# Kernel optimization log

Hardware: AMD Instinct MI355X
Metric: run time of the kernel (lower is better)

Reference implementation:

```python
import jax, jax.numpy as jnp
import numpy as np

N_NODES = 50000
N_EDGES = 800000
D_IN = 128
D_OUT = 128
K = 3


def setup_inputs() -> dict:
    key = jax.random.key(0)
    k1, k2, k3, k4 = jax.random.split(key, 4)
    x = jax.random.normal(k1, (N_NODES, D_IN), dtype=jnp.float32)
    src = jax.random.randint(k2, (N_EDGES,), 0, N_NODES, dtype=jnp.int32)
    dst = jax.random.randint(k3, (N_EDGES,), 0, N_NODES, dtype=jnp.int32)
    edge_index = jnp.stack([src, dst], axis=0)  # [2, E]
    W = jax.random.normal(k4, (D_OUT, D_IN * (K + 1)), dtype=jnp.float32) * 0.02
    b = jnp.zeros((D_OUT,), dtype=jnp.float32)
    return {"x": x, "edge_index": edge_index, "W": W, "b": b}


def _mean_propagate(h, src, dst, n_nodes):
    # scatter-mean: out[v] = mean_{(u,v) in E} h[u]
    msgs = h[src]                                             # [E, D] gather
    summed = jax.ops.segment_sum(msgs, dst, num_segments=n_nodes)
    cnt = jax.ops.segment_sum(jnp.ones((src.shape[0], 1), h.dtype), dst,
                              num_segments=n_nodes)
    return summed / jnp.maximum(cnt, 1.0)


def reference(x, edge_index, W, b):
    src, dst = edge_index[0], edge_index[1]
    n = x.shape[0]
    terms = [x]
    terms.append(_mean_propagate(x, src, dst, n))             # T1 = P x
    for _ in range(K - 1):                                    # T_k = 2 P T_{k-1} - T_{k-2}
        terms.append(2.0 * _mean_propagate(terms[-1], src, dst, n) - terms[-2])
    h = jnp.concatenate(terms, axis=-1)                       # [N, D*(K+1)]
    return h @ W.T + b
```

## Files before the change

### kernel.cpp

```cpp
#include <hip/hip_runtime.h>
#include <stdint.h>

#define D 128
#define LDHB 512
#define MAXD 64
#define FILL_SUB 128

typedef unsigned short u16;
typedef __attribute__((ext_vector_type(8))) short short8;
typedef __attribute__((ext_vector_type(4))) float f32x4;

__device__ __forceinline__ u16 f2bf(float f) {
    uint32_t u = __builtin_bit_cast(uint32_t, f);
    u += 0x7FFFu + ((u >> 16) & 1u);
    return (u16)(u >> 16);
}
__device__ __forceinline__ float bflo(uint32_t w) {
    return __builtin_bit_cast(float, w << 16);
}
__device__ __forceinline__ float bfhi(uint32_t w) {
    return __builtin_bit_cast(float, w & 0xFFFF0000u);
}
__device__ __forceinline__ uint32_t packbf(float lo, float hi) {
    return (uint32_t)f2bf(lo) | ((uint32_t)f2bf(hi) << 16);
}


__global__ void zero_kernel(int* __restrict__ p, int n) {
    int i = blockIdx.x * blockDim.x + threadIdx.x;
    if (i < n) p[i] = 0;
}

__global__ __launch_bounds__(256) void fill_ell_kernel(
        const int* __restrict__ src, const int* __restrict__ dst, int E, int n,
        int* __restrict__ cnt, u16* __restrict__ ell) {
    int grp = blockIdx.x & 7;
    int sub = blockIdx.x >> 3;
    int S = (n + 7) >> 3;
    int lo = grp * S;
    int hi = lo + S; if (hi > n) hi = n;
    const int stride = FILL_SUB * 256;
    for (int i = sub * 256 + (int)threadIdx.x; i < E; i += stride) {
        int d = dst[i];
        if (d >= lo && d < hi) {
            int pos = atomicAdd(&cnt[d], 1);
            if (pos < MAXD) ell[(size_t)d * MAXD + pos] = (u16)src[i];
        }
    }
}


__global__ __launch_bounds__(256) void castx_kernel(const float* __restrict__ x,
                                                    u16* __restrict__ Hb, int n) {
    int gid = blockIdx.x * 256 + threadIdx.x;
    if (gid >= n * 16) return;
    int row = gid >> 4, c8 = (gid & 15) * 8;
    const float4* p = (const float4*)(x + (size_t)row * D + c8);
    float4 f0 = p[0], f1 = p[1];
    uint4 o;
    o.x = packbf(f0.x, f0.y); o.y = packbf(f0.z, f0.w);
    o.z = packbf(f1.x, f1.y); o.w = packbf(f1.z, f1.w);
    *(uint4*)(Hb + (size_t)row * LDHB + c8) = o;
}


__global__ __launch_bounds__(256) void packw_kernel(const float* __restrict__ W,
                                                    u16* __restrict__ Bp) {
    int o = blockIdx.x * 256 + threadIdx.x;
    int kt = o >> 13, rem = o & 8191;
    int j = rem >> 6, w = rem & 63, s2 = w >> 3, e = w & 7;
    int k16 = s2 ^ (j & 7);
    int k = kt * 64 + k16 * 8 + e;
    float val;
    if (k < 128)      val = W[(size_t)j * 512 + k];
    else if (k < 256) val = W[(size_t)j * 512 + k] - W[(size_t)j * 512 + k + 256];
    else if (k < 384) val = W[(size_t)j * 512 + k];
    else              val = 2.0f * W[(size_t)j * 512 + k];
    Bp[o] = f2bf(val);
}


__global__ __launch_bounds__(256) void prop_kernel(u16* Hb, int colin, int colsub,
                                                   float scale, int dosub,
                                                   const int* __restrict__ cnt,
                                                   const u16* __restrict__ ell,
                                                   int colout, int n) {
    int g = blockIdx.x * 16 + ((int)threadIdx.x >> 4);
    if (g >= n) return;
    int lane16 = (int)threadIdx.x & 15;
    int c8 = lane16 * 8;
    int deg = cnt[g];
    if (deg > MAXD) deg = MAXD;
    const u16* row = ell + (size_t)g * MAXD;
    float a0 = 0, a1 = 0, a2 = 0, a3 = 0, a4 = 0, a5 = 0, a6 = 0, a7 = 0;
    for (int base = 0; base < deg; base += 16) {
        int m = deg - base; if (m > 16) m = 16;
        int si = 0;
        if (lane16 < m) si = (int)row[base + lane16];
#pragma unroll 4
        for (int j = 0; j < m; ++j) {
            int s = __shfl(si, j, 16);
            uint4 v = *(const uint4*)(Hb + (size_t)s * LDHB + colin + c8);
            a0 += bflo(v.x); a1 += bfhi(v.x);
            a2 += bflo(v.y); a3 += bfhi(v.y);
            a4 += bflo(v.z); a5 += bfhi(v.z);
            a6 += bflo(v.w); a7 += bfhi(v.w);
        }
    }
    float inv = scale / (float)(deg > 1 ? deg : 1);
    a0 *= inv; a1 *= inv; a2 *= inv; a3 *= inv;
    a4 *= inv; a5 *= inv; a6 *= inv; a7 *= inv;
    if (dosub) {
        uint4 sv = *(const uint4*)(Hb + (size_t)g * LDHB + colsub + c8);
        a0 -= bflo(sv.x); a1 -= bfhi(sv.x);
        a2 -= bflo(sv.y); a3 -= bfhi(sv.y);
        a4 -= bflo(sv.z); a5 -= bfhi(sv.z);
        a6 -= bflo(sv.w); a7 -= bfhi(sv.w);
    }
    uint4 o;
    o.x = packbf(a0, a1); o.y = packbf(a2, a3);
    o.z = packbf(a4, a5); o.w = packbf(a6, a7);
    *(uint4*)(Hb + (size_t)g * LDHB + colout + c8) = o;
}


__global__ __launch_bounds__(256) void gemm_kernel(const u16* __restrict__ Hb,
                                                   const u16* __restrict__ Bp,
                                                   const float* __restrict__ bias,
                                                   float* __restrict__ out, int n) {
    __shared__ uint4 Asm[128 * 8];
    __shared__ uint4 Bsm[128 * 8];

    const int t = (int)threadIdx.x;
    const int wave = t >> 6, lane = t & 63;
    const int wr = wave >> 1, wc = wave & 1;
    const int m0 = blockIdx.x * 128;
    const int lrow = lane & 15, lk = lane >> 4;

    f32x4 acc[4][4];
#pragma unroll
    for (int m = 0; m < 4; ++m)
#pragma unroll
        for (int nf = 0; nf < 4; ++nf) acc[m][nf] = (f32x4)0.0f;

#pragma unroll 1
    for (int kt = 0; kt < 8; ++kt) {
#pragma unroll
        for (int i = 0; i < 4; ++i) {
            int flat = i * 256 + t;
            int row = flat >> 3, c16 = flat & 7;
            int grow = m0 + row;
            uint4 v = make_uint4(0, 0, 0, 0);
            if (grow < n) v = *(const uint4*)(Hb + (size_t)grow * LDHB + kt * 64 + c16 * 8);
            Asm[row * 8 + (c16 ^ (row & 7))] = v;
        }
        const u16* bsrc = Bp + kt * 8192;
#pragma unroll
        for (int i = 0; i < 4; ++i) {
            int flat = i * 256 + t;
            Bsm[flat] = *(const uint4*)(bsrc + flat * 8);
        }
        __syncthreads();

#pragma unroll
        for (int kk2 = 0; kk2 < 2; ++kk2) {
            int k16 = kk2 * 4 + lk;
            short8 af[4], bfv[4];
#pragma unroll
            for (int m = 0; m < 4; ++m) {
                int r = wr * 64 + m * 16 + lrow;
                af[m] = __builtin_bit_cast(short8, Asm[r * 8 + (k16 ^ (r & 7))]);
            }
#pragma unroll
            for (int nf = 0; nf < 4; ++nf) {
                int j = wc * 64 + nf * 16 + lrow;
                bfv[nf] = __builtin_bit_cast(short8, Bsm[j * 8 + (k16 ^ (j & 7))]);
            }
#pragma unroll
            for (int m = 0; m < 4; ++m)
#pragma unroll
                for (int nf = 0; nf < 4; ++nf)
                    acc[m][nf] = __builtin_amdgcn_mfma_f32_16x16x32_bf16(
                        af[m], bfv[nf], acc[m][nf], 0, 0, 0);
        }
        __syncthreads();
    }

#pragma unroll
    for (int nf = 0; nf < 4; ++nf) {
        int j = wc * 64 + nf * 16 + lrow;
        float bj = bias[j];
#pragma unroll
        for (int m = 0; m < 4; ++m) {
            int rbase = m0 + wr * 64 + m * 16 + lk * 4;
#pragma unroll
            for (int q = 0; q < 4; ++q) {
                int row = rbase + q;
                if (row < n) out[(size_t)row * D + j] = acc[m][nf][q] + bj;
            }
        }
    }
}


static inline size_t align_up(size_t x, size_t a) { return (x + a - 1) & ~(a - 1); }

extern "C" void kernel_launch(void* const* d_in, const int* in_sizes, int n_in,
                              void* d_out, int out_size, void* d_ws, size_t ws_size,
                              hipStream_t stream) {
    const float* x  = (const float*)d_in[0];
    const int*   ei = (const int*)d_in[1];
    const float* W  = (const float*)d_in[2];
    const float* b  = (const float*)d_in[3];
    float* out = (float*)d_out;

    const int n = in_sizes[0] / D;
    const int E = in_sizes[1] / 2;
    const int* src = ei;
    const int* dst = ei + E;

    char* w = (char*)d_ws;
    size_t o = 0;
    int* cnt = (int*)(w + o); o = align_up(o + (size_t)n * 4, 256);
    u16* ell = (u16*)(w + o); o = align_up(o + (size_t)n * MAXD * 2, 256);
    u16* Hb  = (u16*)(w + o); o = align_up(o + (size_t)n * LDHB * 2, 256);
    u16* Bp  = (u16*)(w + o); o = align_up(o + (size_t)65536 * 2, 256);
    (void)ws_size;

    zero_kernel<<<(n + 255) / 256, 256, 0, stream>>>(cnt, n);
    fill_ell_kernel<<<8 * FILL_SUB, 256, 0, stream>>>(src, dst, E, n, cnt, ell);

    castx_kernel<<<(n * 16 + 255) / 256, 256, 0, stream>>>(x, Hb, n);
    packw_kernel<<<256, 256, 0, stream>>>(W, Bp);

    const int pgrid = (n + 15) / 16;
    prop_kernel<<<pgrid, 256, 0, stream>>>(Hb, 0,   0,   1.0f, 0, cnt, ell, 128, n);
    prop_kernel<<<pgrid, 256, 0, stream>>>(Hb, 128, 0,   2.0f, 1, cnt, ell, 256, n);
    prop_kernel<<<pgrid, 256, 0, stream>>>(Hb, 256, 0,   1.0f, 0, cnt, ell, 384, n);

    gemm_kernel<<<(n + 127) / 128, 256, 0, stream>>>(Hb, Bp, b, out, n);
}
```

Before: 243.4 us.

## Fold Chebyshev recurrence into weights and pad ELL with sentinel zero row

Rewrites the Chebyshev terms as plain powers of the mean-propagation operator (P x, P² x, P³ x). The recurrence coefficients are folded into the packed weight matrix, so the propagation kernels no longer read and subtract an earlier term. ELL rows are pre-filled with a sentinel index pointing at an extra all-zero row. This lets the gather loop run a fixed, fully unrolled 16-wide batch with vector index loads instead of per-lane shuffles. The cost is an extra sentinel-fill pass over the ELL buffer and redundant gathers of the zero row for the padded slots.

```diff
diff --git a/kernel.cpp b/kernel.cpp
--- a/kernel.cpp
+++ b/kernel.cpp
@@ -24,11 +24,22 @@
 __device__ __forceinline__ uint32_t packbf(float lo, float hi) {
     return (uint32_t)f2bf(lo) | ((uint32_t)f2bf(hi) << 16);
 }
+__device__ __forceinline__ uint32_t sel8(const uint4& a, const uint4& b, int j) {
+    switch (j) {
+        case 0: return a.x; case 1: return a.y; case 2: return a.z; case 3: return a.w;
+        case 4: return b.x; case 5: return b.y; case 6: return b.z; default: return b.w;
+    }
+}
 
 
 __global__ void zero_kernel(int* __restrict__ p, int n) {
     int i = blockIdx.x * blockDim.x + threadIdx.x;
     if (i < n) p[i] = 0;
+}
+
+__global__ void sentinel_kernel(uint4* __restrict__ ell4, int total4, uint32_t pat) {
+    int i = blockIdx.x * blockDim.x + threadIdx.x;
+    if (i < total4) ell4[i] = make_uint4(pat, pat, pat, pat);
 }
 
 __global__ __launch_bounds__(256) void fill_ell_kernel(
@@ -53,14 +64,23 @@
 __global__ __launch_bounds__(256) void castx_kernel(const float* __restrict__ x,
                                                     u16* __restrict__ Hb, int n) {
     int gid = blockIdx.x * 256 + threadIdx.x;
-    if (gid >= n * 16) return;
+    if (gid >= (n + 1) * 16) return;
     int row = gid >> 4, c8 = (gid & 15) * 8;
-    const float4* p = (const float4*)(x + (size_t)row * D + c8);
-    float4 f0 = p[0], f1 = p[1];
     uint4 o;
-    o.x = packbf(f0.x, f0.y); o.y = packbf(f0.z, f0.w);
-    o.z = packbf(f1.x, f1.y); o.w = packbf(f1.z, f1.w);
+    if (row < n) {
+        const float4* p = (const float4*)(x + (size_t)row * D + c8);
+        float4 f0 = p[0], f1 = p[1];
+        o.x = packbf(f0.x, f0.y); o.y = packbf(f0.z, f0.w);
+        o.z = packbf(f1.x, f1.y); o.w = packbf(f1.z, f1.w);
+    } else {
+        o = make_uint4(0, 0, 0, 0);
+    }
     *(uint4*)(Hb + (size_t)row * LDHB + c8) = o;
+}
+
+__global__ void zrow_kernel(u16* __restrict__ Hb, int n) {
+    int i = threadIdx.x;
+    if (i < 48) ((uint4*)(Hb + (size_t)n * LDHB + 128))[i] = make_uint4(0, 0, 0, 0);
 }
 
 
@@ -71,35 +91,34 @@
     int j = rem >> 6, w = rem & 63, s2 = w >> 3, e = w & 7;
     int k16 = s2 ^ (j & 7);
     int k = kt * 64 + k16 * 8 + e;
+    const float* Wj = W + (size_t)j * 512;
     float val;
-    if (k < 128)      val = W[(size_t)j * 512 + k];
-    else if (k < 256) val = W[(size_t)j * 512 + k] - W[(size_t)j * 512 + k + 256];
-    else if (k < 384) val = W[(size_t)j * 512 + k];
-    else              val = 2.0f * W[(size_t)j * 512 + k];
+    if (k < 128)      val = Wj[k] - Wj[k + 256];
+    else if (k < 256) val = Wj[k] - 3.0f * Wj[k + 256];
+    else if (k < 384) val = 2.0f * Wj[k];
+    else              val = 4.0f * Wj[k];
     Bp[o] = f2bf(val);
 }
 
 
-__global__ __launch_bounds__(256) void prop_kernel(u16* Hb, int colin, int colsub,
-                                                   float scale, int dosub,
+__global__ __launch_bounds__(256) void prop_kernel(u16* __restrict__ Hb, int colin,
+                                                   int colout,
                                                    const int* __restrict__ cnt,
                                                    const u16* __restrict__ ell,
-                                                   int colout, int n) {
+                                                   int np) {
     int g = blockIdx.x * 16 + ((int)threadIdx.x >> 4);
-    if (g >= n) return;
-    int lane16 = (int)threadIdx.x & 15;
-    int c8 = lane16 * 8;
+    if (g >= np) return;
+    int c8 = ((int)threadIdx.x & 15) * 8;
     int deg = cnt[g];
     if (deg > MAXD) deg = MAXD;
     const u16* row = ell + (size_t)g * MAXD;
     float a0 = 0, a1 = 0, a2 = 0, a3 = 0, a4 = 0, a5 = 0, a6 = 0, a7 = 0;
     for (int base = 0; base < deg; base += 16) {
-        int m = deg - base; if (m > 16) m = 16;
-        int si = 0;
-        if (lane16 < m) si = (int)row[base + lane16];
-#pragma unroll 4
-        for (int j = 0; j < m; ++j) {
-            int s = __shfl(si, j, 16);
+        uint4 i0 = *(const uint4*)(row + base);
+        uint4 i1 = *(const uint4*)(row + base + 8);
+#pragma unroll
+        for (int j = 0; j < 16; ++j) {
+            int s = (int)((sel8(i0, i1, j >> 1) >> ((j & 1) * 16)) & 0xFFFFu);
             uint4 v = *(const uint4*)(Hb + (size_t)s * LDHB + colin + c8);
             a0 += bflo(v.x); a1 += bfhi(v.x);
             a2 += bflo(v.y); a3 += bfhi(v.y);
@@ -107,19 +126,10 @@
             a6 += bflo(v.w); a7 += bfhi(v.w);
         }
     }
-    float inv = scale / (float)(deg > 1 ? deg : 1);
-    a0 *= inv; a1 *= inv; a2 *= inv; a3 *= inv;
-    a4 *= inv; a5 *= inv; a6 *= inv; a7 *= inv;
-    if (dosub) {
-        uint4 sv = *(const uint4*)(Hb + (size_t)g * LDHB + colsub + c8);
-        a0 -= bflo(sv.x); a1 -= bfhi(sv.x);
-        a2 -= bflo(sv.y); a3 -= bfhi(sv.y);
-        a4 -= bflo(sv.z); a5 -= bfhi(sv.z);
-        a6 -= bflo(sv.w); a7 -= bfhi(sv.w);
-    }
+    float inv = 1.0f / (float)(deg > 1 ? deg : 1);
     uint4 o;
-    o.x = packbf(a0, a1); o.y = packbf(a2, a3);
-    o.z = packbf(a4, a5); o.w = packbf(a6, a7);
+    o.x = packbf(a0 * inv, a1 * inv); o.y = packbf(a2 * inv, a3 * inv);
+    o.z = packbf(a4 * inv, a5 * inv); o.w = packbf(a6 * inv, a7 * inv);
     *(uint4*)(Hb + (size_t)g * LDHB + colout + c8) = o;
 }
 
@@ -218,25 +228,30 @@
     const int E = in_sizes[1] / 2;
     const int* src = ei;
     const int* dst = ei + E;
+    const int np = n + 1;
 
     char* w = (char*)d_ws;
     size_t o = 0;
-    int* cnt = (int*)(w + o); o = align_up(o + (size_t)n * 4, 256);
+    int* cnt = (int*)(w + o); o = align_up(o + (size_t)np * 4, 256);
     u16* ell = (u16*)(w + o); o = align_up(o + (size_t)n * MAXD * 2, 256);
-    u16* Hb  = (u16*)(w + o); o = align_up(o + (size_t)n * LDHB * 2, 256);
+    u16* Hb  = (u16*)(w + o); o = align_up(o + (size_t)np * LDHB * 2, 256);
     u16* Bp  = (u16*)(w + o); o = align_up(o + (size_t)65536 * 2, 256);
     (void)ws_size;
 
-    zero_kernel<<<(n + 255) / 256, 256, 0, stream>>>(cnt, n);
+    zero_kernel<<<(np + 255) / 256, 256, 0, stream>>>(cnt, np);
+    const int total4 = n * MAXD / 8;
+    const uint32_t pat = (uint32_t)n | ((uint32_t)n << 16);
+    sentinel_kernel<<<(total4 + 255) / 256, 256, 0, stream>>>((uint4*)ell, total4, pat);
     fill_ell_kernel<<<8 * FILL_SUB, 256, 0, stream>>>(src, dst, E, n, cnt, ell);
 
-    castx_kernel<<<(n * 16 + 255) / 256, 256, 0, stream>>>(x, Hb, n);
+    castx_kernel<<<(np * 16 + 255) / 256, 256, 0, stream>>>(x, Hb, n);
+    zrow_kernel<<<1, 64, 0, stream>>>(Hb, n);
     packw_kernel<<<256, 256, 0, stream>>>(W, Bp);
 
-    const int pgrid = (n + 15) / 16;
-    prop_kernel<<<pgrid, 256, 0, stream>>>(Hb, 0,   0,   1.0f, 0, cnt, ell, 128, n);
-    prop_kernel<<<pgrid, 256, 0, stream>>>(Hb, 128, 0,   2.0f, 1, cnt, ell, 256, n);
-    prop_kernel<<<pgrid, 256, 0, stream>>>(Hb, 256, 0,   1.0f, 0, cnt, ell, 384, n);
+    const int pgrid = (np + 15) / 16;
+    prop_kernel<<<pgrid, 256, 0, stream>>>(Hb, 0,   128, cnt, ell, np);
+    prop_kernel<<<pgrid, 256, 0, stream>>>(Hb, 128, 256, cnt, ell, np);
+    prop_kernel<<<pgrid, 256, 0, stream>>>(Hb, 256, 384, cnt, ell, np);
 
     gemm_kernel<<<(n + 127) / 128, 256, 0, stream>>>(Hb, Bp, b, out, n);
 }
```

Measured after the change: 235.2 us. 3.4% less time.
